# Kernel tuning notes

Hardware: AMD Instinct MI355X
Metric: run time of the kernel (lower is better)

The kernel has to match this reference:

```python
import jax, jax.numpy as jnp
import numpy as np

D_MODEL = 256      # cfg.d_model
D_INPUT = 64       # cfg.d_input == n_bands
MEM = 10           # cfg.memory_length
NSYNC = 32         # cfg.n_synch_out
ITERS = 2          # cfg.iterations (internal CTM ticks per audio frame)
VOCAB = 15
MINW = 16          # SynapseUNET minimum width; depth=2 -> widths [256, 16]
MHD = 2            # memory_hidden_dims
SYNC_DIM = NSYNC * (NSYNC + 1) // 2  # 528 upper-tri pairwise products


def _ln(x, g, b, eps=1e-5):
    m = x.mean(-1, keepdims=True)
    v = ((x - m) ** 2).mean(-1, keepdims=True)
    return (x - m) * jax.lax.rsqrt(v + eps) * g + b


def _glu(x):
    a, b = jnp.split(x, 2, axis=-1)
    return a * jax.nn.sigmoid(b)


def setup_inputs() -> dict:
    key = jax.random.key(0)
    ks = iter(jax.random.split(key, 40))
    def rn(shape, fan_in):
        return jax.random.uniform(next(ks), shape, jnp.float32, -1.0, 1.0) / np.sqrt(fan_in)
    B, T = 16, 1500
    z = jnp.zeros
    o = jnp.ones
    return {
        "batch_features": jax.random.normal(next(ks), (B, T, D_INPUT), jnp.float32),
        # learned initial traces
        "start_trace": rn((D_MODEL, MEM), MEM),
        "start_activated_trace": rn((D_MODEL, MEM), MEM),
        # classic-control backbone: Linear(64->64) + ReLU
        "Wb": rn((D_INPUT, D_INPUT), D_INPUT), "bb": z((D_INPUT,)),
        # SynapseUNET depth=2, widths [256,16]; input dim = d_input + d_model = 320
        "Wf": rn((D_INPUT + D_MODEL, 2 * D_MODEL), D_INPUT + D_MODEL), "bf": z((2 * D_MODEL,)),
        "gf": o((D_MODEL,)), "bef": z((D_MODEL,)),
        "Wd": rn((D_MODEL, 2 * MINW), D_MODEL), "bd": z((2 * MINW,)),
        "gd": o((MINW,)), "bed": z((MINW,)),
        "Wu": rn((MINW, 2 * D_MODEL), MINW), "bu": z((2 * D_MODEL,)),
        "gu": o((D_MODEL,)), "beu": z((D_MODEL,)),
        "gs": o((D_MODEL,)), "bes": z((D_MODEL,)),
        # deep neuron-level models (per-neuron MLP over the memory trace)
        "w1": rn((MEM, D_MODEL, 2 * MHD), MEM), "b1": z((1, D_MODEL, 2 * MHD)),
        "w2": rn((MHD, D_MODEL, 2), MHD), "b2": z((1, D_MODEL, 2)),
        # output head Linear(528 -> 15)
        "Wh": rn((SYNC_DIM, VOCAB), SYNC_DIM), "bh": z((VOCAB,)),
    }


def reference(batch_features, start_trace, start_activated_trace, Wb, bb,
              Wf, bf, gf, bef, Wd, bd, gd, bed, Wu, bu, gu, beu, gs, bes,
              w1, b1, w2, b2, Wh, bh):
    B = batch_features.shape[0]
    iu, ju = np.triu_indices(NSYNC)  # static index pattern (528 pairs)

    st0 = jnp.broadcast_to(start_trace, (B, D_MODEL, MEM))
    ast0 = jnp.broadcast_to(start_activated_trace, (B, D_MODEL, MEM))

    def synapses(x):  # (B, 320) -> (B, 256), U-Net with one down/up level
        h0 = _ln(_glu(x @ Wf + bf), gf, bef)        # (B, 256)
        d1 = _ln(_glu(h0 @ Wd + bd), gd, bed)       # (B, 16)
        u0 = _ln(_glu(d1 @ Wu + bu), gu, beu)       # (B, 256)
        return _ln(u0 + h0, gs, bes)                # skip + LN

    def nlm(trace):  # per-neuron MLP over memory: (B, 256, 10) -> (B, 256)
        h = _glu(jnp.einsum('bdm,mdh->bdh', trace, w1) + b1)  # (B, 256, 2)
        h = _glu(jnp.einsum('bdm,mdh->bdh', h, w2) + b2)      # (B, 256, 1)
        return h[..., 0]

    def step(carry, x_t):
        st, ast = carry
        kv = jax.nn.relu(x_t @ Wb + bb)  # backbone features (B, 64)
        act = ast[:, :, -1]
        for _ in range(ITERS):  # internal CTM ticks (fixed, small)
            pre = jnp.concatenate([kv, act], axis=-1)             # (B, 320)
            state = synapses(pre)                                  # (B, 256)
            st = jnp.concatenate([st[:, :, 1:], state[:, :, None]], axis=-1)
            act = nlm(st)                                          # (B, 256)
            ast = jnp.concatenate([ast[:, :, 1:], act[:, :, None]], axis=-1)
        sel = act[:, :NSYNC]  # 'first-last': out-sync uses first n_synch_out neurons
        sync = (sel[:, :, None] * sel[:, None, :])[:, iu, ju]      # (B, 528)
        return (st, ast), sync @ Wh + bh                            # (B, 15)

    _, logits = jax.lax.scan(step, (st0, ast0), jnp.swapaxes(batch_features, 0, 1))
    return jnp.swapaxes(logits, 0, 1)  # (B, T, vocab)
```

## Files before the change

kernel.cpp:

```cpp
#include <hip/hip_runtime.h>
#include <math.h>

#define T_LEN 1500
#define DM 256
#define DI 64
#define MEMN 10
#define SYNCD 528
#define VOC 15

typedef _Float16 f16x2 __attribute__((ext_vector_type(2)));
typedef _Float16 f16x8 __attribute__((ext_vector_type(8)));

#define FDOT2(a, b, c) __builtin_amdgcn_fdot2((a), (b), (c), false)

static __device__ __forceinline__ float dot8(f16x8 w, f16x8 q, float acc) {
  acc = FDOT2(__builtin_shufflevector(w, w, 0, 1), __builtin_shufflevector(q, q, 0, 1), acc);
  acc = FDOT2(__builtin_shufflevector(w, w, 2, 3), __builtin_shufflevector(q, q, 2, 3), acc);
  acc = FDOT2(__builtin_shufflevector(w, w, 4, 5), __builtin_shufflevector(q, q, 4, 5), acc);
  acc = FDOT2(__builtin_shufflevector(w, w, 6, 7), __builtin_shufflevector(q, q, 6, 7), acc);
  return acc;
}
static __device__ __forceinline__ f16x2 pack2(float a, float b) {
  f16x2 r; r.x = (_Float16)a; r.y = (_Float16)b; return r;
}
static __device__ __forceinline__ float sigm(float x) { return 1.0f / (1.0f + __expf(-x)); }

#define DPP_TERM(x, ctrl, rmask) \
  __int_as_float(__builtin_amdgcn_update_dpp(0, __float_as_int(x), (ctrl), (rmask), 0xF, true))
#define DPPADD(x, ctrl, rmask) (x) += DPP_TERM(x, ctrl, rmask)
#define WSUM2(a, b) do { \
  DPPADD(a, 0x111, 0xF); DPPADD(b, 0x111, 0xF); \
  DPPADD(a, 0x112, 0xF); DPPADD(b, 0x112, 0xF); \
  DPPADD(a, 0x114, 0xF); DPPADD(b, 0x114, 0xF); \
  DPPADD(a, 0x118, 0xF); DPPADD(b, 0x118, 0xF); \
  DPPADD(a, 0x142, 0xA); DPPADD(b, 0x142, 0xA); \
  DPPADD(a, 0x143, 0xC); DPPADD(b, 0x143, 0xC); \
} while (0)
static __device__ __forceinline__ float readlane_f(float x, int l) {
  return __int_as_float(__builtin_amdgcn_readlane(__float_as_int(x), l));
}

struct Params {
  const float *x, *st0, *ast0, *Wb, *bb, *Wf, *bf, *gf, *bef,
              *Wd, *bd, *gd, *bed, *Wu, *bu, *gu, *beu, *gs, *bes,
              *w1, *b1, *w2, *b2, *Wh, *bh;
  float* out;
};

struct Smem {
  float4 W1v[MEMN * DM];
  float4 W2v[DM];
  float4 B1v[DM];
  float2 B2v[DM];
  float Bf[2 * DM];
  float Bu[2 * DM];
  float Bd[32];
  float Gf[DM], Bef[DM], Gu[DM], Beu[DM], Gs[DM], Bes[DM];
  float Gd[16], Bed[16];
  float Bh[16];
  float Bb[DI];
  __attribute__((aligned(16))) float St[MEMN * DM];
  __attribute__((aligned(16))) float H0[DM];
  float Act[DM];
  __attribute__((aligned(16))) float D1[16];
  float X2[2][DI];
  __attribute__((aligned(16))) f16x2 Pre2[160];
  float PartD[16 * 33];
  float PartK[512];
  float PartH[240];
  float2 RedAB[8];
  float2 Red2AB[8];
  float Prod[SYNCD];
  float WhL[SYNCD * VOC];
  int Pair[SYNCD];
};

#define FOR20(X) X(0) X(1) X(2) X(3) X(4) X(5) X(6) X(7) X(8) X(9) \
                 X(10) X(11) X(12) X(13) X(14) X(15) X(16) X(17) X(18) X(19)

#define DECLW(i) f16x8 wa##i, wb##i;
#define LOADW(i) { const float* Wc = P.Wf + (size_t)(p160 + (i) * 8) * 512 + ch; \
  f16x8 ta, tb; \
  _Pragma("unroll") for (int e = 0; e < 8; ++e) { \
    ta[e] = (_Float16)Wc[e * 512]; tb[e] = (_Float16)Wc[e * 512 + 256]; } \
  wa##i = ta; wb##i = tb; }
#define DOT0(i) { f16x8 q = pr8[i]; aA0 = dot8(wa##i, q, aA0); aB0 = dot8(wb##i, q, aB0); }
#define DOT1(i) { f16x8 q = pr8[i]; aA1 = dot8(wa##i, q, aA1); aB1 = dot8(wb##i, q, aB1); }
#define DOTSEQ DOT0(0) DOT1(1) DOT0(2) DOT1(3) DOT0(4) DOT1(5) DOT0(6) DOT1(7) DOT0(8) DOT1(9) \
               DOT0(10) DOT1(11) DOT0(12) DOT1(13) DOT0(14) DOT1(15) DOT0(16) DOT1(17) DOT0(18) DOT1(19)

__global__ __launch_bounds__(512) __attribute__((amdgpu_waves_per_eu(2, 2)))
void ctm_kernel(Params P) {
  const int tid = threadIdx.x;
  const int b = blockIdx.x;
  __shared__ Smem sm_s;
  Smem* sm = &sm_s;

  for (int i = tid; i < MEMN * DM; i += 512) sm->W1v[i] = ((const float4*)P.w1)[i];
  if (tid < DM) {
    float2 a = ((const float2*)P.w2)[tid];
    float2 c = ((const float2*)P.w2)[DM + tid];
    float4 w; w.x = a.x; w.y = a.y; w.z = c.x; w.w = c.y;
    sm->W2v[tid] = w;
    sm->B1v[tid] = ((const float4*)P.b1)[tid];
    sm->B2v[tid] = ((const float2*)P.b2)[tid];
    sm->Gf[tid] = P.gf[tid]; sm->Bef[tid] = P.bef[tid];
    sm->Gu[tid] = P.gu[tid]; sm->Beu[tid] = P.beu[tid];
    sm->Gs[tid] = P.gs[tid]; sm->Bes[tid] = P.bes[tid];
  }
  sm->Bf[tid] = P.bf[tid];
  sm->Bu[tid] = P.bu[tid];
  if (tid < 32) sm->Bd[tid] = P.bd[tid];
  if (tid < 16) { sm->Gd[tid] = P.gd[tid]; sm->Bed[tid] = P.bed[tid]; }
  if (tid < VOC) sm->Bh[tid] = P.bh[tid];
  if (tid < DI) sm->Bb[tid] = P.bb[tid];
  for (int i = tid; i < MEMN * DM; i += 512) {
    int m = i >> 8, d = i & 255;
    sm->St[m * DM + d] = P.st0[d * MEMN + m];
  }
  if (tid < DI) sm->X2[0][tid] = P.x[(size_t)b * T_LEN * DI + tid];
  for (int i = tid; i < SYNCD * VOC; i += 512) sm->WhL[i] = P.Wh[i];
  for (int pp = tid; pp < SYNCD; pp += 512) {
    int i = 0, cum = 0;
    while (pp >= cum + (32 - i)) { cum += 32 - i; ++i; }
    sm->Pair[pp] = (i << 8) | (i + (pp - cum));
  }

  const int p = tid & 1;
  const int ch = tid >> 1;
  const int p160 = p * 160;
  FOR20(DECLW)
  FOR20(LOADW)
  const int jD = tid & 31, kcD = tid >> 5;
  float wd[16];
  #pragma unroll
  for (int q = 0; q < 16; ++q) wd[q] = P.Wd[(kcD * 16 + q) * 32 + jD];
  float wua[8], wub[8];
  #pragma unroll
  for (int q = 0; q < 8; ++q) {
    wua[q] = P.Wu[(p * 8 + q) * 512 + ch];
    wub[q] = P.Wu[(p * 8 + q) * 512 + ch + 256];
  }
  const int jK = tid & 63, kcK = tid >> 6;
  float wbr[8];
  #pragma unroll
  for (int q = 0; q < 8; ++q) wbr[q] = P.Wb[(kcK * 8 + q) * 64 + jK];

  __syncthreads();

  {
    float s = 0.f;
    #pragma unroll
    for (int q = 0; q < 8; ++q) s += sm->X2[0][kcK * 8 + q] * wbr[q];
    sm->PartK[kcK * 64 + jK] = s;
    if ((tid & 3) == 0) {
      int e = tid >> 2;
      float a0 = P.ast0[(2 * e) * MEMN + (MEMN - 1)];
      float a1 = P.ast0[(2 * e + 1) * MEMN + (MEMN - 1)];
      sm->Pre2[32 + e] = pack2(a0, a1);
    }
  }
  __syncthreads();
  if (tid >= 256 && tid < 320) {
    int j = tid - 256;
    float kv = sm->Bb[j];
    #pragma unroll
    for (int kc = 0; kc < 8; ++kc) kv += sm->PartK[kc * 64 + j];
    kv = fmaxf(kv, 0.f);
    float kn = DPP_TERM(kv, 0xB1, 0xF);
    if ((j & 1) == 0) sm->Pre2[j >> 1] = pack2(kv, kn);
  }
  __syncthreads();

  int head = 0;
  for (int t = 0; t < T_LEN; ++t) {
    float xr = 0.f;
    if (tid < DI && t + 1 < T_LEN) xr = P.x[((size_t)b * T_LEN + (t + 1)) * DI + tid];

    for (int it = 0; it < 2; ++it) {
      if (it == 1 && tid < DI) sm->X2[(t + 1) & 1][tid] = xr;
      float aA0 = 0.f, aA1 = 0.f, aB0 = 0.f, aB1 = 0.f;
      const f16x8* pr8 = (const f16x8*)(sm->Pre2 + p * 80);
      DOTSEQ
      float av = aA0 + aA1, bv = aB0 + aB1;
      DPPADD(av, 0xB1, 0xF);
      DPPADD(bv, 0xB1, 0xF);
      av += sm->Bf[ch]; bv += sm->Bf[DM + ch];
      float g = av * sigm(bv);
      float s1 = g, s2 = g * g;
      WSUM2(s1, s2);
      if ((tid & 63) == 63) { float2 r; r.x = s1; r.y = s2; sm->RedAB[tid >> 6] = r; }
      __syncthreads();

      float S1 = 0.f, S2 = 0.f;
      #pragma unroll
      for (int w = 0; w < 8; ++w) { float2 r = sm->RedAB[w]; S1 += r.x; S2 += r.y; }
      float mean = S1 * (1.0f / 512.0f);
      float var = S2 * (1.0f / 512.0f) - mean * mean;
      float h0v = (g - mean) * rsqrtf(var + 1e-5f) * sm->Gf[ch] + sm->Bef[ch];
      if (!p) sm->H0[ch] = h0v;
      __syncthreads();

      {
        float s = 0.f;
        #pragma unroll
        for (int qq = 0; qq < 4; ++qq) {
          float4 hv = ((const float4*)sm->H0)[kcD * 4 + qq];
          s += hv.x * wd[qq * 4 + 0] + hv.y * wd[qq * 4 + 1]
             + hv.z * wd[qq * 4 + 2] + hv.w * wd[qq * 4 + 3];
        }
        sm->PartD[kcD * 33 + jD] = s;
      }
      __syncthreads();

      if (tid < 32) {
        int j = tid & 15;
        float s = 0.f;
        #pragma unroll
        for (int kc = 0; kc < 16; ++kc) s += sm->PartD[kc * 33 + (tid >> 4) * 16 + j];
        float oth = __shfl_xor(s, 16);
        float gg = (s + sm->Bd[j]) * sigm(oth + sm->Bd[16 + j]);
        float t1 = gg, t2 = gg * gg;
        DPPADD(t1, 0x111, 0xF); DPPADD(t2, 0x111, 0xF);
        DPPADD(t1, 0x112, 0xF); DPPADD(t2, 0x112, 0xF);
        DPPADD(t1, 0x114, 0xF); DPPADD(t2, 0x114, 0xF);
        DPPADD(t1, 0x118, 0xF); DPPADD(t2, 0x118, 0xF);
        float T1 = readlane_f(t1, 15), T2 = readlane_f(t2, 15);
        float mn = T1 * (1.0f / 16.0f), vr = T2 * (1.0f / 16.0f) - mn * mn;
        float d1 = (gg - mn) * rsqrtf(vr + 1e-5f) * sm->Gd[j] + sm->Bed[j];
        if (tid < 16) sm->D1[j] = d1;
      }
      __syncthreads();

      float gu;
      {
        const float4* d4 = (const float4*)sm->D1;
        float4 dl = d4[p * 2], dh = d4[p * 2 + 1];
        float ua = dl.x * wua[0] + dl.y * wua[1] + dl.z * wua[2] + dl.w * wua[3]
                 + dh.x * wua[4] + dh.y * wua[5] + dh.z * wua[6] + dh.w * wua[7];
        float ub = dl.x * wub[0] + dl.y * wub[1] + dl.z * wub[2] + dl.w * wub[3]
                 + dh.x * wub[4] + dh.y * wub[5] + dh.z * wub[6] + dh.w * wub[7];
        DPPADD(ua, 0xB1, 0xF);
        DPPADD(ub, 0xB1, 0xF);
        ua += sm->Bu[ch]; ub += sm->Bu[DM + ch];
        gu = ua * sigm(ub);
        float t1 = gu, t2 = gu * gu;
        WSUM2(t1, t2);
        if ((tid & 63) == 63) { float2 r; r.x = t1; r.y = t2; sm->RedAB[tid >> 6] = r; }
      }
      __syncthreads();

      float x2v;
      {
        float U1 = 0.f, U2 = 0.f;
        #pragma unroll
        for (int w = 0; w < 8; ++w) { float2 r = sm->RedAB[w]; U1 += r.x; U2 += r.y; }
        float mn = U1 * (1.0f / 512.0f), vr = U2 * (1.0f / 512.0f) - mn * mn;
        float u0 = (gu - mn) * rsqrtf(vr + 1e-5f) * sm->Gu[ch] + sm->Beu[ch];
        x2v = u0 + h0v;
        float t1 = x2v, t2 = x2v * x2v;
        WSUM2(t1, t2);
        if ((tid & 63) == 63) { float2 r; r.x = t1; r.y = t2; sm->Red2AB[tid >> 6] = r; }
      }
      __syncthreads();

      {
        float V1 = 0.f, V2 = 0.f;
        #pragma unroll
        for (int w = 0; w < 8; ++w) { float2 r = sm->Red2AB[w]; V1 += r.x; V2 += r.y; }
        float mn = V1 * (1.0f / 512.0f), vr = V2 * (1.0f / 512.0f) - mn * mn;
        float state = (x2v - mn) * rsqrtf(vr + 1e-5f) * sm->Gs[ch] + sm->Bes[ch];
        if (!p) sm->St[head * DM + ch] = state;
        float4 h1 = sm->B1v[ch];
        int base = head + 1; if (base >= MEMN) base -= MEMN;
        #pragma unroll
        for (int m = 0; m < MEMN - 1; ++m) {
          int slot = base + m; if (slot >= MEMN) slot -= MEMN;
          float tr = sm->St[slot * DM + ch];
          float4 wv = sm->W1v[m * DM + ch];
          h1.x += tr * wv.x; h1.y += tr * wv.y; h1.z += tr * wv.z; h1.w += tr * wv.w;
        }
        {
          float4 wv = sm->W1v[(MEMN - 1) * DM + ch];
          h1.x += state * wv.x; h1.y += state * wv.y; h1.z += state * wv.z; h1.w += state * wv.w;
        }
        float g0 = h1.x * sigm(h1.z), g1 = h1.y * sigm(h1.w);
        float4 w2v = sm->W2v[ch];
        float2 b2v = sm->B2v[ch];
        float o0 = g0 * w2v.x + g1 * w2v.z + b2v.x;
        float o1 = g0 * w2v.y + g1 * w2v.w + b2v.y;
        float act = o0 * sigm(o1);
        if (!p) sm->Act[ch] = act;
        float an = DPP_TERM(act, 0x4E, 0xF);
        if ((tid & 3) == 0) sm->Pre2[32 + (tid >> 2)] = pack2(act, an);
        head += 1; if (head >= MEMN) head = 0;
      }
      __syncthreads();
    }

    {
      int pr = sm->Pair[tid];
      sm->Prod[tid] = sm->Act[pr >> 8] * sm->Act[pr & 255];
      if (tid < SYNCD - 512) {
        int pr2 = sm->Pair[512 + tid];
        sm->Prod[512 + tid] = sm->Act[pr2 >> 8] * sm->Act[pr2 & 255];
      }
      const float* X = sm->X2[(t + 1) & 1];
      float s = 0.f;
      #pragma unroll
      for (int q = 0; q < 8; ++q) s += X[kcK * 8 + q] * wbr[q];
      sm->PartK[kcK * 64 + jK] = s;
      if (t > 0 && tid < VOC) {
        float o = sm->Bh[tid];
        #pragma unroll
        for (int kc2 = 0; kc2 < 16; ++kc2) o += sm->PartH[kc2 * 15 + tid];
        P.out[((size_t)b * T_LEN + (t - 1)) * VOC + tid] = o;
      }
    }
    __syncthreads();

    if (tid < 240) {
      int kc = (tid * 4370) >> 16;
      int v = tid - kc * 15;
      float s = 0.f;
      #pragma unroll
      for (int q = 0; q < 33; ++q) {
        int pp = kc * 33 + q;
        s += sm->Prod[pp] * sm->WhL[pp * 15 + v];
      }
      sm->PartH[kc * 15 + v] = s;
    } else if (tid >= 256 && tid < 320) {
      int j = tid - 256;
      float kv = sm->Bb[j];
      #pragma unroll
      for (int kc = 0; kc < 8; ++kc) kv += sm->PartK[kc * 64 + j];
      kv = fmaxf(kv, 0.f);
      float kn = DPP_TERM(kv, 0xB1, 0xF);
      if ((j & 1) == 0) sm->Pre2[j >> 1] = pack2(kv, kn);
    }
    __syncthreads();
  }

  if (tid < VOC) {
    float o = sm->Bh[tid];
    #pragma unroll
    for (int kc = 0; kc < 16; ++kc) o += sm->PartH[kc * 15 + tid];
    P.out[((size_t)b * T_LEN + (T_LEN - 1)) * VOC + tid] = o;
  }
}

extern "C" void kernel_launch(void* const* d_in, const int* in_sizes, int n_in,
                              void* d_out, int out_size, void* d_ws, size_t ws_size,
                              hipStream_t stream) {
  (void)d_ws; (void)ws_size; (void)n_in; (void)out_size;
  Params P;
  P.x   = (const float*)d_in[0];
  P.st0 = (const float*)d_in[1];
  P.ast0= (const float*)d_in[2];
  P.Wb  = (const float*)d_in[3];
  P.bb  = (const float*)d_in[4];
  P.Wf  = (const float*)d_in[5];
  P.bf  = (const float*)d_in[6];
  P.gf  = (const float*)d_in[7];
  P.bef = (const float*)d_in[8];
  P.Wd  = (const float*)d_in[9];
  P.bd  = (const float*)d_in[10];
  P.gd  = (const float*)d_in[11];
  P.bed = (const float*)d_in[12];
  P.Wu  = (const float*)d_in[13];
  P.bu  = (const float*)d_in[14];
  P.gu  = (const float*)d_in[15];
  P.beu = (const float*)d_in[16];
  P.gs  = (const float*)d_in[17];
  P.bes = (const float*)d_in[18];
  P.w1  = (const float*)d_in[19];
  P.b1  = (const float*)d_in[20];
  P.w2  = (const float*)d_in[21];
  P.b2  = (const float*)d_in[22];
  P.Wh  = (const float*)d_in[23];
  P.bh  = (const float*)d_in[24];
  P.out = (float*)d_out;

  int B = in_sizes[0] / (T_LEN * DI);
  hipLaunchKernelGGL(ctm_kernel, dim3(B), dim3(512), 0, stream, P);
}
```

Measured before the change: 12.81 ms.

## Fold first LayerNorm into down-projection and repartition synapse GEMV across 8 lanes

The first synapse matvec is remapped so each thread covers 8 output columns over a 1/8 slice of the input (K split 8 ways). The fp16 weights are pre-packed by a new prep kernel into a workspace layout, and the partial sums are combined with DPP reductions. The LayerNorm before the down projection is folded algebraically: the gamma-scaled GLU output is stored before the mean and variance are known, and the normalisation is applied afterwards using precomputed Wd·gf and Wd·bef vectors. This removes one block-wide barrier per tick. The change adds a second kernel launch each call, and the folded normalisation may round slightly differently.

```diff
diff --git a/kernel.cpp b/kernel.cpp
--- a/kernel.cpp
+++ b/kernel.cpp
@@ -8,6 +8,7 @@
 #define SYNCD 528
 #define VOC 15
 
+typedef _Float16 f16;
 typedef _Float16 f16x2 __attribute__((ext_vector_type(2)));
 typedef _Float16 f16x8 __attribute__((ext_vector_type(8)));
 
@@ -36,6 +37,7 @@
   DPPADD(a, 0x142, 0xA); DPPADD(b, 0x142, 0xA); \
   DPPADD(a, 0x143, 0xC); DPPADD(b, 0x143, 0xC); \
 } while (0)
+#define OSUM(x) do { DPPADD(x, 0xB1, 0xF); DPPADD(x, 0x4E, 0xF); DPPADD(x, 0x141, 0xF); } while (0)
 static __device__ __forceinline__ float readlane_f(float x, int l) {
   return __int_as_float(__builtin_amdgcn_readlane(__float_as_int(x), l));
 }
@@ -44,6 +46,7 @@
   const float *x, *st0, *ast0, *Wb, *bb, *Wf, *bf, *gf, *bef,
               *Wd, *bd, *gd, *bed, *Wu, *bu, *gu, *beu, *gs, *bes,
               *w1, *b1, *w2, *b2, *Wh, *bh;
+  const f16* wf16;
   float* out;
 };
 
@@ -59,8 +62,9 @@
   float Gd[16], Bed[16];
   float Bh[16];
   float Bb[DI];
+  float PC1[32], PC2[32];
   __attribute__((aligned(16))) float St[MEMN * DM];
-  __attribute__((aligned(16))) float H0[DM];
+  __attribute__((aligned(16))) float G[DM];
   float Act[DM];
   __attribute__((aligned(16))) float D1[16];
   float X2[2][DI];
@@ -75,19 +79,30 @@
   int Pair[SYNCD];
 };
 
-#define FOR20(X) X(0) X(1) X(2) X(3) X(4) X(5) X(6) X(7) X(8) X(9) \
-                 X(10) X(11) X(12) X(13) X(14) X(15) X(16) X(17) X(18) X(19)
-
-#define DECLW(i) f16x8 wa##i, wb##i;
-#define LOADW(i) { const float* Wc = P.Wf + (size_t)(p160 + (i) * 8) * 512 + ch; \
-  f16x8 ta, tb; \
-  _Pragma("unroll") for (int e = 0; e < 8; ++e) { \
-    ta[e] = (_Float16)Wc[e * 512]; tb[e] = (_Float16)Wc[e * 512 + 256]; } \
-  wa##i = ta; wb##i = tb; }
-#define DOT0(i) { f16x8 q = pr8[i]; aA0 = dot8(wa##i, q, aA0); aB0 = dot8(wb##i, q, aB0); }
-#define DOT1(i) { f16x8 q = pr8[i]; aA1 = dot8(wa##i, q, aA1); aB1 = dot8(wb##i, q, aB1); }
-#define DOTSEQ DOT0(0) DOT1(1) DOT0(2) DOT1(3) DOT0(4) DOT1(5) DOT0(6) DOT1(7) DOT0(8) DOT1(9) \
-               DOT0(10) DOT1(11) DOT0(12) DOT1(13) DOT0(14) DOT1(15) DOT0(16) DOT1(17) DOT0(18) DOT1(19)
+__global__ __launch_bounds__(512) void wf16_kernel(const float* __restrict__ Wf,
+                                                   f16* __restrict__ out) {
+  int k = blockIdx.x;
+  int c = threadIdx.x;
+  int nk;
+  if (k < 64) nk = k;
+  else { int ch = k - 64; int mc = ch & 63; int j = ch >> 6;
+         nk = 64 + 2 * mc + 128 * (j >> 1) + (j & 1); }
+  out[((size_t)(nk >> 3) * 512 + (size_t)c) * 8 + (nk & 7)] = (f16)Wf[(size_t)k * 512 + c];
+}
+
+#define FOR8K(X) X(0) X(1) X(2) X(3) X(4) X(5) X(6) X(7)
+#define DECLW(K) f16x8 w##K##_0, w##K##_1, w##K##_2, w##K##_3, w##K##_4;
+#define LOADW(K) { size_t cb = (size_t)(mc + 64 * (K)); \
+  w##K##_0 = wf8[(size_t)(5 * o + 0) * 512 + cb]; \
+  w##K##_1 = wf8[(size_t)(5 * o + 1) * 512 + cb]; \
+  w##K##_2 = wf8[(size_t)(5 * o + 2) * 512 + cb]; \
+  w##K##_3 = wf8[(size_t)(5 * o + 3) * 512 + cb]; \
+  w##K##_4 = wf8[(size_t)(5 * o + 4) * 512 + cb]; }
+#define DOTJ(J) { f16x8 q_ = pr8[5 * o + (J)]; \
+  ac0 = dot8(w0_##J, q_, ac0); ac1 = dot8(w1_##J, q_, ac1); \
+  ac2 = dot8(w2_##J, q_, ac2); ac3 = dot8(w3_##J, q_, ac3); \
+  ac4 = dot8(w4_##J, q_, ac4); ac5 = dot8(w5_##J, q_, ac5); \
+  ac6 = dot8(w6_##J, q_, ac6); ac7 = dot8(w7_##J, q_, ac7); }
 
 __global__ __launch_bounds__(512) __attribute__((amdgpu_waves_per_eu(2, 2)))
 void ctm_kernel(Params P) {
@@ -114,9 +129,19 @@
   if (tid < 16) { sm->Gd[tid] = P.gd[tid]; sm->Bed[tid] = P.bed[tid]; }
   if (tid < VOC) sm->Bh[tid] = P.bh[tid];
   if (tid < DI) sm->Bb[tid] = P.bb[tid];
+  if (tid >= 64 && tid < 96) {
+    int j = tid - 64;
+    float pc1 = 0.f, pc2 = 0.f;
+    for (int k = 0; k < 256; ++k) {
+      float w = P.Wd[k * 32 + j];
+      pc1 += P.bef[k] * w;
+      pc2 += P.gf[k] * w;
+    }
+    sm->PC1[j] = pc1; sm->PC2[j] = pc2;
+  }
   for (int i = tid; i < MEMN * DM; i += 512) {
-    int m = i >> 8, d = i & 255;
-    sm->St[m * DM + d] = P.st0[d * MEMN + m];
+    int mm = i >> 8, d = i & 255;
+    sm->St[mm * DM + d] = P.st0[d * MEMN + mm];
   }
   if (tid < DI) sm->X2[0][tid] = P.x[(size_t)b * T_LEN * DI + tid];
   for (int i = tid; i < SYNCD * VOC; i += 512) sm->WhL[i] = P.Wh[i];
@@ -125,16 +150,24 @@
     while (pp >= cum + (32 - i)) { cum += 32 - i; ++i; }
     sm->Pair[pp] = (i << 8) | (i + (pp - cum));
   }
-
-  const int p = tid & 1;
-  const int ch = tid >> 1;
-  const int p160 = p * 160;
-  FOR20(DECLW)
-  FOR20(LOADW)
+  if (tid < 128) {
+    int mc = tid & 63, bb_ = tid >> 6;
+    float a0 = P.ast0[(mc + 128 * bb_) * MEMN + (MEMN - 1)];
+    float a1 = P.ast0[(mc + 64 + 128 * bb_) * MEMN + (MEMN - 1)];
+    sm->Pre2[32 + mc + 64 * bb_] = pack2(a0, a1);
+  }
+
+  const int o = tid & 7;
+  const int mc = tid >> 3;
+  const int ch = mc + 64 * ((tid >> 1) & 3);
+  const f16x8* wf8 = (const f16x8*)P.wf16;
+  FOR8K(DECLW)
+  FOR8K(LOADW)
   const int jD = tid & 31, kcD = tid >> 5;
   float wd[16];
   #pragma unroll
   for (int q = 0; q < 16; ++q) wd[q] = P.Wd[(kcD * 16 + q) * 32 + jD];
+  const int p = tid & 1;
   float wua[8], wub[8];
   #pragma unroll
   for (int q = 0; q < 8; ++q) {
@@ -153,12 +186,6 @@
     #pragma unroll
     for (int q = 0; q < 8; ++q) s += sm->X2[0][kcK * 8 + q] * wbr[q];
     sm->PartK[kcK * 64 + jK] = s;
-    if ((tid & 3) == 0) {
-      int e = tid >> 2;
-      float a0 = P.ast0[(2 * e) * MEMN + (MEMN - 1)];
-      float a1 = P.ast0[(2 * e + 1) * MEMN + (MEMN - 1)];
-      sm->Pre2[32 + e] = pack2(a0, a1);
-    }
   }
   __syncthreads();
   if (tid >= 256 && tid < 320) {
@@ -175,37 +202,41 @@
   int head = 0;
   for (int t = 0; t < T_LEN; ++t) {
     float xr = 0.f;
-    if (tid < DI && t + 1 < T_LEN) xr = P.x[((size_t)b * T_LEN + (t + 1)) * DI + tid];
 
     for (int it = 0; it < 2; ++it) {
       if (it == 1 && tid < DI) sm->X2[(t + 1) & 1][tid] = xr;
-      float aA0 = 0.f, aA1 = 0.f, aB0 = 0.f, aB1 = 0.f;
-      const f16x8* pr8 = (const f16x8*)(sm->Pre2 + p * 80);
-      DOTSEQ
-      float av = aA0 + aA1, bv = aB0 + aB1;
-      DPPADD(av, 0xB1, 0xF);
-      DPPADD(bv, 0xB1, 0xF);
-      av += sm->Bf[ch]; bv += sm->Bf[DM + ch];
-      float g = av * sigm(bv);
+      float ac0 = 0.f, ac1 = 0.f, ac2 = 0.f, ac3 = 0.f;
+      float ac4 = 0.f, ac5 = 0.f, ac6 = 0.f, ac7 = 0.f;
+      const f16x8* pr8 = (const f16x8*)sm->Pre2;
+      DOTJ(0) DOTJ(1) DOTJ(2) DOTJ(3) DOTJ(4)
+      OSUM(ac0); OSUM(ac1); OSUM(ac2); OSUM(ac3);
+      OSUM(ac4); OSUM(ac5); OSUM(ac6); OSUM(ac7);
+      float aa = (tid & 4) ? ((tid & 2) ? ac3 : ac2) : ((tid & 2) ? ac1 : ac0);
+      float bb_ = (tid & 4) ? ((tid & 2) ? ac7 : ac6) : ((tid & 2) ? ac5 : ac4);
+      aa += sm->Bf[ch]; bb_ += sm->Bf[DM + ch];
+      float g = aa * sigm(bb_);
+      float gf_c = sm->Gf[ch];
+      float ghat = g * gf_c;
+      if ((tid & 1) == 0) sm->G[ch] = ghat;
       float s1 = g, s2 = g * g;
       WSUM2(s1, s2);
       if ((tid & 63) == 63) { float2 r; r.x = s1; r.y = s2; sm->RedAB[tid >> 6] = r; }
       __syncthreads();
 
+      if (it == 0 && tid < DI && t + 1 < T_LEN)
+        xr = P.x[((size_t)b * T_LEN + (t + 1)) * DI + tid];
       float S1 = 0.f, S2 = 0.f;
       #pragma unroll
       for (int w = 0; w < 8; ++w) { float2 r = sm->RedAB[w]; S1 += r.x; S2 += r.y; }
-      float mean = S1 * (1.0f / 512.0f);
-      float var = S2 * (1.0f / 512.0f) - mean * mean;
-      float h0v = (g - mean) * rsqrtf(var + 1e-5f) * sm->Gf[ch] + sm->Bef[ch];
-      if (!p) sm->H0[ch] = h0v;
-      __syncthreads();
-
+      float mean_f = S1 * (1.0f / 512.0f);
+      float var_f = S2 * (1.0f / 512.0f) - mean_f * mean_f;
+      float r_f = rsqrtf(var_f + 1e-5f);
+      float h0v = (g - mean_f) * r_f * gf_c + sm->Bef[ch];
       {
         float s = 0.f;
         #pragma unroll
         for (int qq = 0; qq < 4; ++qq) {
-          float4 hv = ((const float4*)sm->H0)[kcD * 4 + qq];
+          float4 hv = ((const float4*)sm->G)[kcD * 4 + qq];
           s += hv.x * wd[qq * 4 + 0] + hv.y * wd[qq * 4 + 1]
              + hv.z * wd[qq * 4 + 2] + hv.w * wd[qq * 4 + 3];
         }
@@ -214,12 +245,12 @@
       __syncthreads();
 
       if (tid < 32) {
-        int j = tid & 15;
-        float s = 0.f;
-        #pragma unroll
-        for (int kc = 0; kc < 16; ++kc) s += sm->PartD[kc * 33 + (tid >> 4) * 16 + j];
-        float oth = __shfl_xor(s, 16);
-        float gg = (s + sm->Bd[j]) * sigm(oth + sm->Bd[16 + j]);
+        float S = 0.f;
+        #pragma unroll
+        for (int kc = 0; kc < 16; ++kc) S += sm->PartD[kc * 33 + tid];
+        float raw = r_f * S - mean_f * r_f * sm->PC2[tid] + sm->PC1[tid] + sm->Bd[tid];
+        float oth = __shfl_xor(raw, 16);
+        float gg = raw * sigm(oth);
         float t1 = gg, t2 = gg * gg;
         DPPADD(t1, 0x111, 0xF); DPPADD(t2, 0x111, 0xF);
         DPPADD(t1, 0x112, 0xF); DPPADD(t2, 0x112, 0xF);
@@ -227,8 +258,8 @@
         DPPADD(t1, 0x118, 0xF); DPPADD(t2, 0x118, 0xF);
         float T1 = readlane_f(t1, 15), T2 = readlane_f(t2, 15);
         float mn = T1 * (1.0f / 16.0f), vr = T2 * (1.0f / 16.0f) - mn * mn;
-        float d1 = (gg - mn) * rsqrtf(vr + 1e-5f) * sm->Gd[j] + sm->Bed[j];
-        if (tid < 16) sm->D1[j] = d1;
+        float d1 = (gg - mn) * rsqrtf(vr + 1e-5f) * sm->Gd[tid & 15] + sm->Bed[tid & 15];
+        if (tid < 16) sm->D1[tid] = d1;
       }
       __syncthreads();
 
@@ -270,14 +301,14 @@
         for (int w = 0; w < 8; ++w) { float2 r = sm->Red2AB[w]; V1 += r.x; V2 += r.y; }
         float mn = V1 * (1.0f / 512.0f), vr = V2 * (1.0f / 512.0f) - mn * mn;
         float state = (x2v - mn) * rsqrtf(vr + 1e-5f) * sm->Gs[ch] + sm->Bes[ch];
-        if (!p) sm->St[head * DM + ch] = state;
+        if ((tid & 1) == 0) sm->St[head * DM + ch] = state;
         float4 h1 = sm->B1v[ch];
         int base = head + 1; if (base >= MEMN) base -= MEMN;
         #pragma unroll
-        for (int m = 0; m < MEMN - 1; ++m) {
-          int slot = base + m; if (slot >= MEMN) slot -= MEMN;
+        for (int mm = 0; mm < MEMN - 1; ++mm) {
+          int slot = base + mm; if (slot >= MEMN) slot -= MEMN;
           float tr = sm->St[slot * DM + ch];
-          float4 wv = sm->W1v[m * DM + ch];
+          float4 wv = sm->W1v[mm * DM + ch];
           h1.x += tr * wv.x; h1.y += tr * wv.y; h1.z += tr * wv.z; h1.w += tr * wv.w;
         }
         {
@@ -290,9 +321,10 @@
         float o0 = g0 * w2v.x + g1 * w2v.z + b2v.x;
         float o1 = g0 * w2v.y + g1 * w2v.w + b2v.y;
         float act = o0 * sigm(o1);
-        if (!p) sm->Act[ch] = act;
-        float an = DPP_TERM(act, 0x4E, 0xF);
-        if ((tid & 3) == 0) sm->Pre2[32 + (tid >> 2)] = pack2(act, an);
+        if ((tid & 1) == 0) sm->Act[ch] = act;
+        float apart = DPP_TERM(act, 0x4E, 0xF);
+        if (o == 0) sm->Pre2[32 + mc] = pack2(act, apart);
+        if (o == 4) sm->Pre2[32 + 64 + mc] = pack2(act, apart);
         head += 1; if (head >= MEMN) head = 0;
       }
       __syncthreads();
@@ -311,10 +343,10 @@
       for (int q = 0; q < 8; ++q) s += X[kcK * 8 + q] * wbr[q];
       sm->PartK[kcK * 64 + jK] = s;
       if (t > 0 && tid < VOC) {
-        float o = sm->Bh[tid];
-        #pragma unroll
-        for (int kc2 = 0; kc2 < 16; ++kc2) o += sm->PartH[kc2 * 15 + tid];
-        P.out[((size_t)b * T_LEN + (t - 1)) * VOC + tid] = o;
+        float o_ = sm->Bh[tid];
+        #pragma unroll
+        for (int kc2 = 0; kc2 < 16; ++kc2) o_ += sm->PartH[kc2 * 15 + tid];
+        P.out[((size_t)b * T_LEN + (t - 1)) * VOC + tid] = o_;
       }
     }
     __syncthreads();
@@ -342,17 +374,17 @@
   }
 
   if (tid < VOC) {
-    float o = sm->Bh[tid];
+    float o_ = sm->Bh[tid];
     #pragma unroll
-    for (int kc = 0; kc < 16; ++kc) o += sm->PartH[kc * 15 + tid];
-    P.out[((size_t)b * T_LEN + (T_LEN - 1)) * VOC + tid] = o;
+    for (int kc = 0; kc < 16; ++kc) o_ += sm->PartH[kc * 15 + tid];
+    P.out[((size_t)b * T_LEN + (T_LEN - 1)) * VOC + tid] = o_;
   }
 }
 
 extern "C" void kernel_launch(void* const* d_in, const int* in_sizes, int n_in,
                               void* d_out, int out_size, void* d_ws, size_t ws_size,
                               hipStream_t stream) {
-  (void)d_ws; (void)ws_size; (void)n_in; (void)out_size;
+  (void)n_in; (void)out_size; (void)ws_size;
   Params P;
   P.x   = (const float*)d_in[0];
   P.st0 = (const float*)d_in[1];
@@ -381,6 +413,10 @@
   P.bh  = (const float*)d_in[24];
   P.out = (float*)d_out;
 
+  f16* wf16 = (f16*)d_ws;
+  hipLaunchKernelGGL(wf16_kernel, dim3(320), dim3(512), 0, stream, P.Wf, wf16);
+  P.wf16 = wf16;
+
   int B = in_sizes[0] / (T_LEN * DI);
   hipLaunchKernelGGL(ctm_kernel, dim3(B), dim3(512), 0, stream, P);
 }
```

After: 14.03 ms. 9.5% more time.

## Fold LayerNorm into down-projection and overlap head/backbone with CTM ticks

Applied to the files above, without the earlier changes.

Rewrites the first LayerNorm plus Wd projection algebraically: the un-normalised, gain-scaled GLU output is written directly and the mean/rsqrt correction is applied afterwards using precomputed Wd·bef and Wd·gf vectors, which removes one barrier per tick. The sync-product, output-head and backbone stages are moved into the slack of the two CTM ticks (delayed by one timestep), removing the two extra barriers at the end of each timestep. The trade is slightly different numerics from the folded LayerNorm and more complex cross-timestep state.

```diff
diff --git a/kernel.cpp b/kernel.cpp
--- a/kernel.cpp
+++ b/kernel.cpp
@@ -59,8 +59,9 @@
   float Gd[16], Bed[16];
   float Bh[16];
   float Bb[DI];
+  float PC1[32], PC2[32];
   __attribute__((aligned(16))) float St[MEMN * DM];
-  __attribute__((aligned(16))) float H0[DM];
+  __attribute__((aligned(16))) float G[DM];
   float Act[DM];
   __attribute__((aligned(16))) float D1[16];
   float X2[2][DI];
@@ -107,6 +108,7 @@
     sm->Gf[tid] = P.gf[tid]; sm->Bef[tid] = P.bef[tid];
     sm->Gu[tid] = P.gu[tid]; sm->Beu[tid] = P.beu[tid];
     sm->Gs[tid] = P.gs[tid]; sm->Bes[tid] = P.bes[tid];
+    sm->Act[tid] = P.ast0[tid * MEMN + (MEMN - 1)];
   }
   sm->Bf[tid] = P.bf[tid];
   sm->Bu[tid] = P.bu[tid];
@@ -114,9 +116,19 @@
   if (tid < 16) { sm->Gd[tid] = P.gd[tid]; sm->Bed[tid] = P.bed[tid]; }
   if (tid < VOC) sm->Bh[tid] = P.bh[tid];
   if (tid < DI) sm->Bb[tid] = P.bb[tid];
+  if (tid >= 64 && tid < 96) {
+    int j = tid - 64;
+    float pc1 = 0.f, pc2 = 0.f;
+    for (int k = 0; k < 256; ++k) {
+      float w = P.Wd[k * 32 + j];
+      pc1 += P.bef[k] * w;
+      pc2 += P.gf[k] * w;
+    }
+    sm->PC1[j] = pc1; sm->PC2[j] = pc2;
+  }
   for (int i = tid; i < MEMN * DM; i += 512) {
-    int m = i >> 8, d = i & 255;
-    sm->St[m * DM + d] = P.st0[d * MEMN + m];
+    int mm = i >> 8, d = i & 255;
+    sm->St[mm * DM + d] = P.st0[d * MEMN + mm];
   }
   if (tid < DI) sm->X2[0][tid] = P.x[(size_t)b * T_LEN * DI + tid];
   for (int i = tid; i < SYNCD * VOC; i += 512) sm->WhL[i] = P.Wh[i];
@@ -124,6 +136,12 @@
     int i = 0, cum = 0;
     while (pp >= cum + (32 - i)) { cum += 32 - i; ++i; }
     sm->Pair[pp] = (i << 8) | (i + (pp - cum));
+  }
+  if ((tid & 3) == 0) {
+    int e = tid >> 2;
+    float a0 = P.ast0[(2 * e) * MEMN + (MEMN - 1)];
+    float a1 = P.ast0[(2 * e + 1) * MEMN + (MEMN - 1)];
+    sm->Pre2[32 + e] = pack2(a0, a1);
   }
 
   const int p = tid & 1;
@@ -153,12 +171,6 @@
     #pragma unroll
     for (int q = 0; q < 8; ++q) s += sm->X2[0][kcK * 8 + q] * wbr[q];
     sm->PartK[kcK * 64 + jK] = s;
-    if ((tid & 3) == 0) {
-      int e = tid >> 2;
-      float a0 = P.ast0[(2 * e) * MEMN + (MEMN - 1)];
-      float a1 = P.ast0[(2 * e + 1) * MEMN + (MEMN - 1)];
-      sm->Pre2[32 + e] = pack2(a0, a1);
-    }
   }
   __syncthreads();
   if (tid >= 256 && tid < 320) {
@@ -179,6 +191,14 @@
 
     for (int it = 0; it < 2; ++it) {
       if (it == 1 && tid < DI) sm->X2[(t + 1) & 1][tid] = xr;
+      if (it == 0 && t > 0) {
+        int pr = sm->Pair[tid];
+        sm->Prod[tid] = sm->Act[pr >> 8] * sm->Act[pr & 255];
+        if (tid < SYNCD - 512) {
+          int pr2 = sm->Pair[512 + tid];
+          sm->Prod[512 + tid] = sm->Act[pr2 >> 8] * sm->Act[pr2 & 255];
+        }
+      }
       float aA0 = 0.f, aA1 = 0.f, aB0 = 0.f, aB1 = 0.f;
       const f16x8* pr8 = (const f16x8*)(sm->Pre2 + p * 80);
       DOTSEQ
@@ -187,6 +207,8 @@
       DPPADD(bv, 0xB1, 0xF);
       av += sm->Bf[ch]; bv += sm->Bf[DM + ch];
       float g = av * sigm(bv);
+      float gf_c = sm->Gf[ch];
+      if (!p) sm->G[ch] = g * gf_c;
       float s1 = g, s2 = g * g;
       WSUM2(s1, s2);
       if ((tid & 63) == 63) { float2 r; r.x = s1; r.y = s2; sm->RedAB[tid >> 6] = r; }
@@ -195,31 +217,48 @@
       float S1 = 0.f, S2 = 0.f;
       #pragma unroll
       for (int w = 0; w < 8; ++w) { float2 r = sm->RedAB[w]; S1 += r.x; S2 += r.y; }
-      float mean = S1 * (1.0f / 512.0f);
-      float var = S2 * (1.0f / 512.0f) - mean * mean;
-      float h0v = (g - mean) * rsqrtf(var + 1e-5f) * sm->Gf[ch] + sm->Bef[ch];
-      if (!p) sm->H0[ch] = h0v;
-      __syncthreads();
-
+      float mean_f = S1 * (1.0f / 512.0f);
+      float var_f = S2 * (1.0f / 512.0f) - mean_f * mean_f;
+      float r_f = rsqrtf(var_f + 1e-5f);
+      float h0v = (g - mean_f) * r_f * gf_c + sm->Bef[ch];
       {
         float s = 0.f;
         #pragma unroll
         for (int qq = 0; qq < 4; ++qq) {
-          float4 hv = ((const float4*)sm->H0)[kcD * 4 + qq];
+          float4 hv = ((const float4*)sm->G)[kcD * 4 + qq];
           s += hv.x * wd[qq * 4 + 0] + hv.y * wd[qq * 4 + 1]
              + hv.z * wd[qq * 4 + 2] + hv.w * wd[qq * 4 + 3];
         }
         sm->PartD[kcD * 33 + jD] = s;
       }
+      if (it == 0) {
+        if (t > 0 && tid < 240) {
+          int kc = (tid * 4370) >> 16;
+          int v = tid - kc * 15;
+          float s = 0.f;
+          #pragma unroll
+          for (int q = 0; q < 33; ++q) {
+            int pp = kc * 33 + q;
+            s += sm->Prod[pp] * sm->WhL[pp * 15 + v];
+          }
+          sm->PartH[kc * 15 + v] = s;
+        }
+      } else {
+        const float* X = sm->X2[(t + 1) & 1];
+        float s = 0.f;
+        #pragma unroll
+        for (int q = 0; q < 8; ++q) s += X[kcK * 8 + q] * wbr[q];
+        sm->PartK[kcK * 64 + jK] = s;
+      }
       __syncthreads();
 
       if (tid < 32) {
-        int j = tid & 15;
-        float s = 0.f;
-        #pragma unroll
-        for (int kc = 0; kc < 16; ++kc) s += sm->PartD[kc * 33 + (tid >> 4) * 16 + j];
-        float oth = __shfl_xor(s, 16);
-        float gg = (s + sm->Bd[j]) * sigm(oth + sm->Bd[16 + j]);
+        float S = 0.f;
+        #pragma unroll
+        for (int kc = 0; kc < 16; ++kc) S += sm->PartD[kc * 33 + tid];
+        float raw = r_f * S - mean_f * r_f * sm->PC2[tid] + sm->PC1[tid] + sm->Bd[tid];
+        float oth = __shfl_xor(raw, 16);
+        float gg = raw * sigm(oth);
         float t1 = gg, t2 = gg * gg;
         DPPADD(t1, 0x111, 0xF); DPPADD(t2, 0x111, 0xF);
         DPPADD(t1, 0x112, 0xF); DPPADD(t2, 0x112, 0xF);
@@ -227,8 +266,14 @@
         DPPADD(t1, 0x118, 0xF); DPPADD(t2, 0x118, 0xF);
         float T1 = readlane_f(t1, 15), T2 = readlane_f(t2, 15);
         float mn = T1 * (1.0f / 16.0f), vr = T2 * (1.0f / 16.0f) - mn * mn;
-        float d1 = (gg - mn) * rsqrtf(vr + 1e-5f) * sm->Gd[j] + sm->Bed[j];
-        if (tid < 16) sm->D1[j] = d1;
+        float d1 = (gg - mn) * rsqrtf(vr + 1e-5f) * sm->Gd[tid & 15] + sm->Bed[tid & 15];
+        if (tid < 16) sm->D1[tid] = d1;
+      } else if (it == 0 && t > 0 && tid >= 64 && tid < 64 + VOC) {
+        int j = tid - 64;
+        float o_ = sm->Bh[j];
+        #pragma unroll
+        for (int kc = 0; kc < 16; ++kc) o_ += sm->PartH[kc * 15 + j];
+        P.out[((size_t)b * T_LEN + (t - 1)) * VOC + j] = o_;
       }
       __syncthreads();
 
@@ -274,10 +319,10 @@
         float4 h1 = sm->B1v[ch];
         int base = head + 1; if (base >= MEMN) base -= MEMN;
         #pragma unroll
-        for (int m = 0; m < MEMN - 1; ++m) {
-          int slot = base + m; if (slot >= MEMN) slot -= MEMN;
+        for (int mm = 0; mm < MEMN - 1; ++mm) {
+          int slot = base + mm; if (slot >= MEMN) slot -= MEMN;
           float tr = sm->St[slot * DM + ch];
-          float4 wv = sm->W1v[m * DM + ch];
+          float4 wv = sm->W1v[mm * DM + ch];
           h1.x += tr * wv.x; h1.y += tr * wv.y; h1.z += tr * wv.z; h1.w += tr * wv.w;
         }
         {
@@ -290,62 +335,52 @@
         float o0 = g0 * w2v.x + g1 * w2v.z + b2v.x;
         float o1 = g0 * w2v.y + g1 * w2v.w + b2v.y;
         float act = o0 * sigm(o1);
-        if (!p) sm->Act[ch] = act;
         float an = DPP_TERM(act, 0x4E, 0xF);
         if ((tid & 3) == 0) sm->Pre2[32 + (tid >> 2)] = pack2(act, an);
+        if (it == 1) {
+          if (!p) sm->Act[ch] = act;
+          if (tid >= 256 && tid < 320) {
+            int j = tid - 256;
+            float kv = sm->Bb[j];
+            #pragma unroll
+            for (int kc = 0; kc < 8; ++kc) kv += sm->PartK[kc * 64 + j];
+            kv = fmaxf(kv, 0.f);
+            float kn = DPP_TERM(kv, 0xB1, 0xF);
+            if ((j & 1) == 0) sm->Pre2[j >> 1] = pack2(kv, kn);
+          }
+        }
         head += 1; if (head >= MEMN) head = 0;
       }
       __syncthreads();
     }
-
-    {
-      int pr = sm->Pair[tid];
-      sm->Prod[tid] = sm->Act[pr >> 8] * sm->Act[pr & 255];
-      if (tid < SYNCD - 512) {
-        int pr2 = sm->Pair[512 + tid];
-        sm->Prod[512 + tid] = sm->Act[pr2 >> 8] * sm->Act[pr2 & 255];
-      }
-      const float* X = sm->X2[(t + 1) & 1];
-      float s = 0.f;
-      #pragma unroll
-      for (int q = 0; q < 8; ++q) s += X[kcK * 8 + q] * wbr[q];
-      sm->PartK[kcK * 64 + jK] = s;
-      if (t > 0 && tid < VOC) {
-        float o = sm->Bh[tid];
-        #pragma unroll
-        for (int kc2 = 0; kc2 < 16; ++kc2) o += sm->PartH[kc2 * 15 + tid];
-        P.out[((size_t)b * T_LEN + (t - 1)) * VOC + tid] = o;
-      }
+  }
+
+  {
+    int pr = sm->Pair[tid];
+    sm->Prod[tid] = sm->Act[pr >> 8] * sm->Act[pr & 255];
+    if (tid < SYNCD - 512) {
+      int pr2 = sm->Pair[512 + tid];
+      sm->Prod[512 + tid] = sm->Act[pr2 >> 8] * sm->Act[pr2 & 255];
     }
-    __syncthreads();
-
-    if (tid < 240) {
-      int kc = (tid * 4370) >> 16;
-      int v = tid - kc * 15;
-      float s = 0.f;
-      #pragma unroll
-      for (int q = 0; q < 33; ++q) {
-        int pp = kc * 33 + q;
-        s += sm->Prod[pp] * sm->WhL[pp * 15 + v];
-      }
-      sm->PartH[kc * 15 + v] = s;
-    } else if (tid >= 256 && tid < 320) {
-      int j = tid - 256;
-      float kv = sm->Bb[j];
-      #pragma unroll
-      for (int kc = 0; kc < 8; ++kc) kv += sm->PartK[kc * 64 + j];
-      kv = fmaxf(kv, 0.f);
-      float kn = DPP_TERM(kv, 0xB1, 0xF);
-      if ((j & 1) == 0) sm->Pre2[j >> 1] = pack2(kv, kn);
+  }
+  __syncthreads();
+  if (tid < 240) {
+    int kc = (tid * 4370) >> 16;
+    int v = tid - kc * 15;
+    float s = 0.f;
+    #pragma unroll
+    for (int q = 0; q < 33; ++q) {
+      int pp = kc * 33 + q;
+      s += sm->Prod[pp] * sm->WhL[pp * 15 + v];
     }
-    __syncthreads();
-  }
-
+    sm->PartH[kc * 15 + v] = s;
+  }
+  __syncthreads();
   if (tid < VOC) {
-    float o = sm->Bh[tid];
+    float o_ = sm->Bh[tid];
     #pragma unroll
-    for (int kc = 0; kc < 16; ++kc) o += sm->PartH[kc * 15 + tid];
-    P.out[((size_t)b * T_LEN + (T_LEN - 1)) * VOC + tid] = o;
+    for (int kc = 0; kc < 16; ++kc) o_ += sm->PartH[kc * 15 + tid];
+    P.out[((size_t)b * T_LEN + (T_LEN - 1)) * VOC + tid] = o_;
   }
 }
 
```

Result: slower. 15.26 ms (+19.1%).

## Fold first LayerNorm into down-projection and drop two barriers per tick

Applied to the files above, without the earlier changes.

The LayerNorm after the first GLU is applied algebraically: the down-projection is computed on gf-scaled raw activations in parallel with the mean/variance reduction, then corrected using precomputed Wd·gf and Wd·bef column sums. The 256→32 reduction now happens across 32 lanes with DPP instead of a shared-memory partial buffer plus a single-warp finish. The small 16-wide LayerNorm is recomputed redundantly by every thread in the up-projection stage. Together these remove two block-wide barriers per internal tick, which matters because the time loop is serial and latency-bound. The cost is some numerical drift from the rearranged sums and a bit of redundant arithmetic per thread.

```diff
diff --git a/kernel.cpp b/kernel.cpp
--- a/kernel.cpp
+++ b/kernel.cpp
@@ -35,6 +35,13 @@
   DPPADD(a, 0x118, 0xF); DPPADD(b, 0x118, 0xF); \
   DPPADD(a, 0x142, 0xA); DPPADD(b, 0x142, 0xA); \
   DPPADD(a, 0x143, 0xC); DPPADD(b, 0x143, 0xC); \
+} while (0)
+#define HSUM2(a, b) do { \
+  DPPADD(a, 0x111, 0xF); DPPADD(b, 0x111, 0xF); \
+  DPPADD(a, 0x112, 0xF); DPPADD(b, 0x112, 0xF); \
+  DPPADD(a, 0x114, 0xF); DPPADD(b, 0x114, 0xF); \
+  DPPADD(a, 0x118, 0xF); DPPADD(b, 0x118, 0xF); \
+  DPPADD(a, 0x142, 0xA); DPPADD(b, 0x142, 0xA); \
 } while (0)
 static __device__ __forceinline__ float readlane_f(float x, int l) {
   return __int_as_float(__builtin_amdgcn_readlane(__float_as_int(x), l));
@@ -59,13 +66,13 @@
   float Gd[16], Bed[16];
   float Bh[16];
   float Bb[DI];
+  float PC1[32], PC2[32];
   __attribute__((aligned(16))) float St[MEMN * DM];
-  __attribute__((aligned(16))) float H0[DM];
+  __attribute__((aligned(16))) float G[DM];
+  __attribute__((aligned(16))) float GG[16];
   float Act[DM];
-  __attribute__((aligned(16))) float D1[16];
   float X2[2][DI];
   __attribute__((aligned(16))) f16x2 Pre2[160];
-  float PartD[16 * 33];
   float PartK[512];
   float PartH[240];
   float2 RedAB[8];
@@ -114,6 +121,16 @@
   if (tid < 16) { sm->Gd[tid] = P.gd[tid]; sm->Bed[tid] = P.bed[tid]; }
   if (tid < VOC) sm->Bh[tid] = P.bh[tid];
   if (tid < DI) sm->Bb[tid] = P.bb[tid];
+  if (tid >= 64 && tid < 96) {
+    int j = tid - 64;
+    float pc1 = 0.f, pc2 = 0.f;
+    for (int k = 0; k < 256; ++k) {
+      float w = P.Wd[k * 32 + j];
+      pc1 += P.bef[k] * w;
+      pc2 += P.gf[k] * w;
+    }
+    sm->PC1[j] = pc1; sm->PC2[j] = pc2;
+  }
   for (int i = tid; i < MEMN * DM; i += 512) {
     int m = i >> 8, d = i & 255;
     sm->St[m * DM + d] = P.st0[d * MEMN + m];
@@ -125,16 +142,25 @@
     while (pp >= cum + (32 - i)) { cum += 32 - i; ++i; }
     sm->Pair[pp] = (i << 8) | (i + (pp - cum));
   }
+  if ((tid & 3) == 0) {
+    int e = tid >> 2;
+    float a0 = P.ast0[(2 * e) * MEMN + (MEMN - 1)];
+    float a1 = P.ast0[(2 * e + 1) * MEMN + (MEMN - 1)];
+    sm->Pre2[32 + e] = pack2(a0, a1);
+  }
 
   const int p = tid & 1;
   const int ch = tid >> 1;
   const int p160 = p * 160;
   FOR20(DECLW)
   FOR20(LOADW)
-  const int jD = tid & 31, kcD = tid >> 5;
-  float wd[16];
+  const int jp = tid >> 5, kcD = tid & 31;
+  float wdA[8], wdB[8];
   #pragma unroll
-  for (int q = 0; q < 16; ++q) wd[q] = P.Wd[(kcD * 16 + q) * 32 + jD];
+  for (int q = 0; q < 8; ++q) {
+    wdA[q] = P.Wd[(kcD * 8 + q) * 32 + jp];
+    wdB[q] = P.Wd[(kcD * 8 + q) * 32 + jp + 16];
+  }
   float wua[8], wub[8];
   #pragma unroll
   for (int q = 0; q < 8; ++q) {
@@ -153,12 +179,6 @@
     #pragma unroll
     for (int q = 0; q < 8; ++q) s += sm->X2[0][kcK * 8 + q] * wbr[q];
     sm->PartK[kcK * 64 + jK] = s;
-    if ((tid & 3) == 0) {
-      int e = tid >> 2;
-      float a0 = P.ast0[(2 * e) * MEMN + (MEMN - 1)];
-      float a1 = P.ast0[(2 * e + 1) * MEMN + (MEMN - 1)];
-      sm->Pre2[32 + e] = pack2(a0, a1);
-    }
   }
   __syncthreads();
   if (tid >= 256 && tid < 320) {
@@ -187,6 +207,8 @@
       DPPADD(bv, 0xB1, 0xF);
       av += sm->Bf[ch]; bv += sm->Bf[DM + ch];
       float g = av * sigm(bv);
+      float gf_c = sm->Gf[ch];
+      if (!p) sm->G[ch] = g * gf_c;
       float s1 = g, s2 = g * g;
       WSUM2(s1, s2);
       if ((tid & 63) == 63) { float2 r; r.x = s1; r.y = s2; sm->RedAB[tid >> 6] = r; }
@@ -195,51 +217,56 @@
       float S1 = 0.f, S2 = 0.f;
       #pragma unroll
       for (int w = 0; w < 8; ++w) { float2 r = sm->RedAB[w]; S1 += r.x; S2 += r.y; }
-      float mean = S1 * (1.0f / 512.0f);
-      float var = S2 * (1.0f / 512.0f) - mean * mean;
-      float h0v = (g - mean) * rsqrtf(var + 1e-5f) * sm->Gf[ch] + sm->Bef[ch];
-      if (!p) sm->H0[ch] = h0v;
-      __syncthreads();
-
+      float mean_f = S1 * (1.0f / 512.0f);
+      float var_f = S2 * (1.0f / 512.0f) - mean_f * mean_f;
+      float r_f = rsqrtf(var_f + 1e-5f);
+      float h0v = (g - mean_f) * r_f * gf_c + sm->Bef[ch];
       {
-        float s = 0.f;
-        #pragma unroll
-        for (int qq = 0; qq < 4; ++qq) {
-          float4 hv = ((const float4*)sm->H0)[kcD * 4 + qq];
-          s += hv.x * wd[qq * 4 + 0] + hv.y * wd[qq * 4 + 1]
-             + hv.z * wd[qq * 4 + 2] + hv.w * wd[qq * 4 + 3];
-        }
-        sm->PartD[kcD * 33 + jD] = s;
-      }
-      __syncthreads();
-
-      if (tid < 32) {
-        int j = tid & 15;
-        float s = 0.f;
-        #pragma unroll
-        for (int kc = 0; kc < 16; ++kc) s += sm->PartD[kc * 33 + (tid >> 4) * 16 + j];
-        float oth = __shfl_xor(s, 16);
-        float gg = (s + sm->Bd[j]) * sigm(oth + sm->Bd[16 + j]);
-        float t1 = gg, t2 = gg * gg;
-        DPPADD(t1, 0x111, 0xF); DPPADD(t2, 0x111, 0xF);
-        DPPADD(t1, 0x112, 0xF); DPPADD(t2, 0x112, 0xF);
-        DPPADD(t1, 0x114, 0xF); DPPADD(t2, 0x114, 0xF);
-        DPPADD(t1, 0x118, 0xF); DPPADD(t2, 0x118, 0xF);
-        float T1 = readlane_f(t1, 15), T2 = readlane_f(t2, 15);
-        float mn = T1 * (1.0f / 16.0f), vr = T2 * (1.0f / 16.0f) - mn * mn;
-        float d1 = (gg - mn) * rsqrtf(vr + 1e-5f) * sm->Gd[j] + sm->Bed[j];
-        if (tid < 16) sm->D1[j] = d1;
+        float4 g0 = ((const float4*)sm->G)[kcD * 2];
+        float4 g1 = ((const float4*)sm->G)[kcD * 2 + 1];
+        float sA = g0.x * wdA[0] + g0.y * wdA[1] + g0.z * wdA[2] + g0.w * wdA[3]
+                 + g1.x * wdA[4] + g1.y * wdA[5] + g1.z * wdA[6] + g1.w * wdA[7];
+        float sB = g0.x * wdB[0] + g0.y * wdB[1] + g0.z * wdB[2] + g0.w * wdB[3]
+                 + g1.x * wdB[4] + g1.y * wdB[5] + g1.z * wdB[6] + g1.w * wdB[7];
+        HSUM2(sA, sB);
+        float rawA = r_f * sA - mean_f * r_f * sm->PC2[jp] + sm->PC1[jp] + sm->Bd[jp];
+        float rawB = r_f * sB - mean_f * r_f * sm->PC2[jp + 16] + sm->PC1[jp + 16] + sm->Bd[16 + jp];
+        float gg = rawA * sigm(rawB);
+        if ((tid & 31) == 31) sm->GG[jp] = gg;
       }
       __syncthreads();
 
       float gu;
       {
-        const float4* d4 = (const float4*)sm->D1;
-        float4 dl = d4[p * 2], dh = d4[p * 2 + 1];
-        float ua = dl.x * wua[0] + dl.y * wua[1] + dl.z * wua[2] + dl.w * wua[3]
-                 + dh.x * wua[4] + dh.y * wua[5] + dh.z * wua[6] + dh.w * wua[7];
-        float ub = dl.x * wub[0] + dl.y * wub[1] + dl.z * wub[2] + dl.w * wub[3]
-                 + dh.x * wub[4] + dh.y * wub[5] + dh.z * wub[6] + dh.w * wub[7];
+        const float4* GG4 = (const float4*)sm->GG;
+        float4 q0 = GG4[0], q1 = GG4[1], q2 = GG4[2], q3 = GG4[3];
+        float sum = q0.x + q0.y + q0.z + q0.w + q1.x + q1.y + q1.z + q1.w
+                  + q2.x + q2.y + q2.z + q2.w + q3.x + q3.y + q3.z + q3.w;
+        float sq = q0.x * q0.x + q0.y * q0.y + q0.z * q0.z + q0.w * q0.w
+                 + q1.x * q1.x + q1.y * q1.y + q1.z * q1.z + q1.w * q1.w
+                 + q2.x * q2.x + q2.y * q2.y + q2.z * q2.z + q2.w * q2.w
+                 + q3.x * q3.x + q3.y * q3.y + q3.z * q3.z + q3.w * q3.w;
+        float mn = sum * (1.0f / 16.0f);
+        float vr = sq * (1.0f / 16.0f) - mn * mn;
+        float rs = rsqrtf(vr + 1e-5f);
+        float4 ga = p ? q2 : q0;
+        float4 gb = p ? q3 : q1;
+        float4 gd0 = ((const float4*)sm->Gd)[p * 2];
+        float4 gd1 = ((const float4*)sm->Gd)[p * 2 + 1];
+        float4 be0 = ((const float4*)sm->Bed)[p * 2];
+        float4 be1 = ((const float4*)sm->Bed)[p * 2 + 1];
+        float d0 = (ga.x - mn) * rs * gd0.x + be0.x;
+        float d1_ = (ga.y - mn) * rs * gd0.y + be0.y;
+        float d2 = (ga.z - mn) * rs * gd0.z + be0.z;
+        float d3 = (ga.w - mn) * rs * gd0.w + be0.w;
+        float d4 = (gb.x - mn) * rs * gd1.x + be1.x;
+        float d5 = (gb.y - mn) * rs * gd1.y + be1.y;
+        float d6 = (gb.z - mn) * rs * gd1.z + be1.z;
+        float d7 = (gb.w - mn) * rs * gd1.w + be1.w;
+        float ua = d0 * wua[0] + d1_ * wua[1] + d2 * wua[2] + d3 * wua[3]
+                 + d4 * wua[4] + d5 * wua[5] + d6 * wua[6] + d7 * wua[7];
+        float ub = d0 * wub[0] + d1_ * wub[1] + d2 * wub[2] + d3 * wub[3]
+                 + d4 * wub[4] + d5 * wub[5] + d6 * wub[6] + d7 * wub[7];
         DPPADD(ua, 0xB1, 0xF);
         DPPADD(ub, 0xB1, 0xF);
         ua += sm->Bu[ch]; ub += sm->Bu[DM + ch];
```

After: 16.08 ms. +25.5%, slower.
